# Kernel optimization log

Hardware: AMD Instinct MI355X
Metric: run time of the kernel (lower is better)

The kernel has to match this reference:

```python
import jax, jax.numpy as jnp
import numpy as np

DIM = 1024
HEADS = 16
HEAD_DIM = DIM // HEADS
FFN = 4 * DIM
EPS = 1e-5


def layer_norm(x, g, b):
    mu = jnp.mean(x, axis=-1, keepdims=True)
    var = jnp.mean(jnp.square(x - mu), axis=-1, keepdims=True)
    return (x - mu) * jax.lax.rsqrt(var + EPS) * g + b


def setup_inputs() -> dict:
    key = jax.random.key(0)
    ks = jax.random.split(key, 12)
    s_d = 1.0 / np.sqrt(DIM)
    s_f = 1.0 / np.sqrt(FFN)
    return {
        "x": jax.random.normal(ks[0], (2, 2048, DIM), dtype=jnp.float32),
        "ln1_g": jnp.ones((DIM,), jnp.float32),
        "ln1_b": jnp.zeros((DIM,), jnp.float32),
        "q_w": jax.random.normal(ks[1], (DIM, DIM), jnp.float32) * s_d,
        "k_w": jax.random.normal(ks[2], (DIM, DIM), jnp.float32) * s_d,
        "v_w": jax.random.normal(ks[3], (DIM, DIM), jnp.float32) * s_d,
        "o_w": jax.random.normal(ks[4], (DIM, DIM), jnp.float32) * s_d,
        "ln2_g": jnp.ones((DIM,), jnp.float32),
        "ln2_b": jnp.zeros((DIM,), jnp.float32),
        "ffn_in_w": jax.random.normal(ks[5], (FFN, DIM), jnp.float32) * s_d,
        "ffn_in_b": jnp.zeros((FFN,), jnp.float32),
        "sw_w": jax.random.normal(ks[6], (FFN, FFN), jnp.float32) * s_f,
        "sw_v": jax.random.normal(ks[7], (FFN, FFN), jnp.float32) * s_f,
        "ffn_out_w": jax.random.normal(ks[8], (DIM, FFN), jnp.float32) * s_f,
        "ffn_out_b": jnp.zeros((DIM,), jnp.float32),
    }


def reference(x, ln1_g, ln1_b, q_w, k_w, v_w, o_w, ln2_g, ln2_b,
              ffn_in_w, ffn_in_b, sw_w, sw_v, ffn_out_w, ffn_out_b):
    B, L, D = x.shape
    scale = HEAD_DIM ** -0.5

    # --- attention block ---
    h = layer_norm(x, ln1_g, ln1_b)
    q = (h @ q_w.T).reshape(B, L, HEADS, HEAD_DIM).transpose(0, 2, 1, 3)
    k = (h @ k_w.T).reshape(B, L, HEADS, HEAD_DIM).transpose(0, 2, 1, 3)
    v = (h @ v_w.T).reshape(B, L, HEADS, HEAD_DIM).transpose(0, 2, 1, 3)
    attn = jnp.einsum("bhqd,bhkd->bhqk", q, k) * scale
    attn = jax.nn.softmax(attn, axis=-1)
    out = jnp.einsum("bhqk,bhkd->bhqd", attn, v)
    out = out.transpose(0, 2, 1, 3).reshape(B, L, D)
    x = x + out @ o_w.T

    # --- FFN block: Linear -> SwiGLU -> Linear ---
    h = layer_norm(x, ln2_g, ln2_b)
    u = h @ ffn_in_w.T + ffn_in_b                 # [B,L,FFN]
    g = jax.nn.silu(u @ sw_w.T) * (u @ sw_v.T)    # SwiGLU
    x = x + g @ ffn_out_w.T + ffn_out_b
    return x
```

## Files before the change

### kernel.cpp

```cpp
#include <hip/hip_runtime.h>
#include <hip/hip_bf16.h>

#define TOK 4096
#define DIM 1024
#define FFN_N 4096
#define SEQ 2048
#define HD 64

using short8 = __attribute__((ext_vector_type(8))) short;
using short4v = __attribute__((ext_vector_type(4))) short;
using f32x4 = __attribute__((ext_vector_type(4))) float;

__device__ __forceinline__ short f2b(float f){
  return __builtin_bit_cast(short, __float2bfloat16(f));
}
__device__ __forceinline__ float b2f(short s){
  return __bfloat162float(__builtin_bit_cast(__hip_bfloat16, s));
}
__device__ __forceinline__ unsigned cvtpk(float lo, float hi){
  unsigned r;
  asm("v_cvt_pk_bf16_f32 %0, %1, %2" : "=v"(r) : "v"(lo), "v"(hi));
  return r;
}

__device__ __forceinline__ void gl_lds16(const short* g, short* l){
  __builtin_amdgcn_global_load_lds(
      (const __attribute__((address_space(1))) unsigned int*)g,
      (__attribute__((address_space(3))) unsigned int*)l, 16, 0, 0);
}

#define BARRAW() asm volatile("s_barrier" ::: "memory")
#define VMCNT(n) asm volatile("s_waitcnt vmcnt(" #n ")" ::: "memory")

__global__ __launch_bounds__(256) void castk(const float* __restrict__ src,
                                             short* __restrict__ dst, int n){
  int stride = gridDim.x*256*4;
  for (int i = (blockIdx.x*256 + threadIdx.x)*4; i < n; i += stride){
    float4 v = *reinterpret_cast<const float4*>(src + i);
    short4v o; o[0]=f2b(v.x); o[1]=f2b(v.y); o[2]=f2b(v.z); o[3]=f2b(v.w);
    *reinterpret_cast<short4v*>(dst + i) = o;
  }
}

__global__ __launch_bounds__(256) void lnk(const float* __restrict__ x,
                                           const float* __restrict__ g,
                                           const float* __restrict__ b,
                                           short* __restrict__ out){
  int row = blockIdx.x;
  int t = threadIdx.x;
  const float* xr = x + (size_t)row*DIM;
  float4 v = *reinterpret_cast<const float4*>(xr + t*4);
  float s = v.x+v.y+v.z+v.w;
  float s2 = v.x*v.x+v.y*v.y+v.z*v.z+v.w*v.w;
  #pragma unroll
  for (int off=1; off<64; off<<=1){ s += __shfl_xor(s,off); s2 += __shfl_xor(s2,off); }
  __shared__ float as_[4], as2_[4];
  if ((t&63)==0){ as_[t>>6]=s; as2_[t>>6]=s2; }
  __syncthreads();
  s = as_[0]+as_[1]+as_[2]+as_[3];
  s2 = as2_[0]+as2_[1]+as2_[2]+as2_[3];
  float mu = s * (1.0f/DIM);
  float var = s2 * (1.0f/DIM) - mu*mu;
  float r = rsqrtf(var + 1e-5f);
  float4 gv = *reinterpret_cast<const float4*>(g + t*4);
  float4 bv = *reinterpret_cast<const float4*>(b + t*4);
  short4v o;
  o[0]=f2b((v.x-mu)*r*gv.x + bv.x);
  o[1]=f2b((v.y-mu)*r*gv.y + bv.y);
  o[2]=f2b((v.z-mu)*r*gv.z + bv.z);
  o[3]=f2b((v.w-mu)*r*gv.w + bv.w);
  *reinterpret_cast<short4v*>(out + (size_t)row*DIM + t*4) = o;
}

template<int MODE>
__global__ __launch_bounds__(256,2) void gemm_bt(
    const short* __restrict__ A, const short* __restrict__ Bt,
    short* __restrict__ Cb, float* __restrict__ Cf,
    const float* __restrict__ bias, const float* __restrict__ resid,
    const short* __restrict__ aux,
    int M, int N, int K)
{
  __shared__ __align__(16) short Al[128*32];
  __shared__ __align__(16) short Bl[128*32];
  const int tid = threadIdx.x, lane = tid & 63, w = tid >> 6;
  const int wr = w >> 1, wc = w & 1;
  const int bx = blockIdx.x, by = blockIdx.y;

  const short* ga0 = A  + (size_t)(by*128 + w*32 + (lane>>2))*K + (lane&3)*8;
  const short* gb0 = Bt + (size_t)(bx*128 + w*32 + (lane>>2))*K + (lane&3)*8;
  short* la0 = &Al[w*32*32];
  short* lb0 = &Bl[w*32*32];

  f32x4 acc[4][4] = {};

  for (int k0 = 0; k0 < K; k0 += 32){
    __syncthreads();
    gl_lds16(ga0 + k0,                 la0);
    gl_lds16(ga0 + k0 + (size_t)16*K,  la0 + 16*32);
    gl_lds16(gb0 + k0,                 lb0);
    gl_lds16(gb0 + k0 + (size_t)16*K,  lb0 + 16*32);
    __syncthreads();
    short8 af[4], bf[4];
    #pragma unroll
    for (int m=0;m<4;m++)
      af[m] = *reinterpret_cast<const short8*>(&Al[(wr*64 + m*16 + (lane&15))*32 + (lane>>4)*8]);
    #pragma unroll
    for (int n=0;n<4;n++)
      bf[n] = *reinterpret_cast<const short8*>(&Bl[(wc*64 + n*16 + (lane&15))*32 + (lane>>4)*8]);
    #pragma unroll
    for (int m=0;m<4;m++)
      #pragma unroll
      for (int n=0;n<4;n++)
        acc[m][n] = __builtin_amdgcn_mfma_f32_16x16x32_bf16(af[m], bf[n], acc[m][n], 0,0,0);
  }

  #pragma unroll
  for (int m=0;m<4;m++){
    #pragma unroll
    for (int n=0;n<4;n++){
      #pragma unroll
      for (int j=0;j<4;j++){
        int r = by*128 + wr*64 + m*16 + ((lane>>4)<<2) + j;
        int c = bx*128 + wc*64 + n*16 + (lane&15);
        float v = acc[m][n][j];
        if (MODE==1 || MODE==3) v += bias[c];
        size_t idx = (size_t)r*N + c;
        if (MODE==4){
          float a = b2f(aux[idx]);
          float sg = a / (1.0f + __expf(-a));
          Cb[idx] = f2b(sg * v);
        } else if (MODE<=1) {
          Cb[idx] = f2b(v);
        } else {
          Cf[idx] = resid[idx] + v;
        }
      }
    }
  }
}

template<int MODE>
__global__ __launch_bounds__(512,2) void gemm256(
    const short* __restrict__ A, const short* __restrict__ Bt,
    short* __restrict__ Cb,
    const float* __restrict__ bias, const short* __restrict__ aux,
    int M, int N, int K)
{
  __shared__ __align__(16) short L[65536];
  const int tid = threadIdx.x, lane = tid&63, w = tid>>6;
  const int q15 = lane&15, h8 = lane>>4;
  const int wm = w>>2, wn = w&3;
  const int NT = K>>6;

  int bid = blockIdx.x;
  int wg = (bid&7)*(gridDim.x>>3) + (bid>>3);
  const int by = wg >> 4, bx = wg & 15;

  const int isub = w*8 + (lane>>3);
  const int koff = ((lane&7) ^ ((lane>>3)&7))*8;

  const short* gA[2][2]; const short* gB[2][2];
  #pragma unroll
  for (int hh=0; hh<2; hh++){
    #pragma unroll
    for (int j=0; j<2; j++){
      int i = j*64 + isub;
      int Ra = by*256 + (i>>6)*128 + hh*64 + (i&63);
      gA[hh][j] = A + (size_t)Ra*K + koff;
      int Rb = bx*256 + (i>>5)*64 + hh*32 + (i&31);
      gB[hh][j] = Bt + (size_t)Rb*K + koff;
    }
  }

  auto stA = [&](int db, int hh, int j, int kt){
    gl_lds16(gA[hh][j] + (size_t)kt*64, &L[db*32768 + hh*8192 + j*4096 + w*512]);
  };
  auto stB = [&](int db, int hh, int j, int kt){
    gl_lds16(gB[hh][j] + (size_t)kt*64, &L[db*32768 + (2+hh)*8192 + j*4096 + w*512]);
  };
  auto rdA = [&](int db, int mh, int m, int ks)->short8{
    int i = wm*64 + m*16 + q15;
    int ch = (ks*4 + h8) ^ (i&7);
    return *reinterpret_cast<const short8*>(&L[db*32768 + mh*8192 + i*64 + ch*8]);
  };
  auto rdB = [&](int db, int nh, int n, int ks)->short8{
    int i = wn*32 + n*16 + q15;
    int ch = (ks*4 + h8) ^ (i&7);
    return *reinterpret_cast<const short8*>(&L[db*32768 + (2+nh)*8192 + i*64 + ch*8]);
  };

  f32x4 acc[8][4] = {};
  short8 af[4][2], bf[2][2];

#define MFMA_QUAD(MH, NH)                                                      \
  __builtin_amdgcn_s_setprio(1);                                               \
  _Pragma("unroll")                                                            \
  for (int m=0;m<4;m++){                                                       \
    _Pragma("unroll")                                                          \
    for (int n=0;n<2;n++){                                                     \
      acc[(MH)*4+m][(NH)*2+n] = __builtin_amdgcn_mfma_f32_16x16x32_bf16(       \
          af[m][0], bf[n][0], acc[(MH)*4+m][(NH)*2+n], 0,0,0);                 \
      acc[(MH)*4+m][(NH)*2+n] = __builtin_amdgcn_mfma_f32_16x16x32_bf16(       \
          af[m][1], bf[n][1], acc[(MH)*4+m][(NH)*2+n], 0,0,0);                 \
    }                                                                          \
  }                                                                            \
  __builtin_amdgcn_s_setprio(0);

  stA(0,0,0,0); stA(0,0,1,0);
  stB(0,0,0,0); stB(0,0,1,0);
  stA(0,1,0,0); stA(0,1,1,0);
  stB(0,1,0,0); stB(0,1,1,0);
  VMCNT(4);
  BARRAW();

  for (int t = 0; t < NT; ++t){
    const int db = t&1;
    const bool pf = (t+1 < NT);

    #pragma unroll
    for (int m=0;m<4;m++){ af[m][0]=rdA(db,0,m,0); af[m][1]=rdA(db,0,m,1); }
    #pragma unroll
    for (int n=0;n<2;n++){ bf[n][0]=rdB(db,0,n,0); bf[n][1]=rdB(db,0,n,1); }
    if (pf){ stA(db^1,0,0,t+1); stA(db^1,0,1,t+1); }
    BARRAW();
    MFMA_QUAD(0,0);
    if (pf){ VMCNT(2); } else { VMCNT(0); }
    BARRAW();

    #pragma unroll
    for (int n=0;n<2;n++){ bf[n][0]=rdB(db,1,n,0); bf[n][1]=rdB(db,1,n,1); }
    if (pf){ stB(db^1,0,0,t+1); stB(db^1,0,1,t+1); }
    BARRAW();
    MFMA_QUAD(0,1);
    BARRAW();

    #pragma unroll
    for (int m=0;m<4;m++){ af[m][0]=rdA(db,1,m,0); af[m][1]=rdA(db,1,m,1); }
    if (pf){ stA(db^1,1,0,t+1); stA(db^1,1,1,t+1); }
    BARRAW();
    MFMA_QUAD(1,1);
    BARRAW();

    #pragma unroll
    for (int n=0;n<2;n++){ bf[n][0]=rdB(db,0,n,0); bf[n][1]=rdB(db,0,n,1); }
    if (pf){ stB(db^1,1,0,t+1); stB(db^1,1,1,t+1); }
    BARRAW();
    MFMA_QUAD(1,0);
    if (pf){ VMCNT(4); }
    BARRAW();
  }

  #pragma unroll
  for (int mq=0;mq<8;mq++){
    #pragma unroll
    for (int nq=0;nq<4;nq++){
      #pragma unroll
      for (int jj=0;jj<4;jj++){
        int r = by*256 + wm*128 + mq*16 + h8*4 + jj;
        int c = bx*256 + wn*64  + nq*16 + q15;
        float v = acc[mq][nq][jj];
        if (MODE==1) v += bias[c];
        size_t idx = (size_t)r*N + c;
        if (MODE==4){
          float a = b2f(aux[idx]);
          float sg = a / (1.0f + __expf(-a));
          Cb[idx] = f2b(sg * v);
        } else {
          Cb[idx] = f2b(v);
        }
      }
    }
  }
#undef MFMA_QUAD
}

__global__ __launch_bounds__(256) void vtrk(const short* __restrict__ V,
                                            short* __restrict__ Vt){
  __shared__ __align__(16) short T[64*72];
  const int tid = threadIdx.x;
  const int bh = blockIdx.y;
  const int b = bh >> 4, hd = bh & 15;
  const int t0 = blockIdx.x * 64;
  const short* src = V + (size_t)b*SEQ*DIM + (size_t)hd*HD;

  const int r = tid>>2, c = tid&3;
  short8 a0 = *reinterpret_cast<const short8*>(src + (size_t)(t0+r)*DIM + c*8);
  short8 a1 = *reinterpret_cast<const short8*>(src + (size_t)(t0+r)*DIM + (c+4)*8);
  *reinterpret_cast<short8*>(&T[r*72 + c*8]) = a0;
  *reinterpret_cast<short8*>(&T[r*72 + (c+4)*8]) = a1;
  __syncthreads();

  short* dst = Vt + (size_t)bh*HD*SEQ;
  #pragma unroll
  for (int dd=0; dd<2; dd++){
    int d = (tid>>3) + dd*32;
    int tc = tid&7;
    short8 o;
    #pragma unroll
    for (int j=0;j<8;j++) o[j] = T[(tc*8+j)*72 + d];
    *reinterpret_cast<short8*>(dst + (size_t)d*SEQ + t0 + tc*8) = o;
  }
}

__global__ __launch_bounds__(256) void attnk(
    const short* __restrict__ Q, const short* __restrict__ K,
    const short* __restrict__ Vt, short* __restrict__ O)
{
  __shared__ __align__(16) short Kl[64*64];
  __shared__ __align__(16) short Vl[64*64];
  __shared__ __align__(16) short Pl[4*16*72];

  const int tid = threadIdx.x, lane = tid&63, w = tid>>6;
  const int h = lane>>4, q15 = lane&15;
  const int bh = blockIdx.y;
  const int b = bh >> 4, hd = bh & 15;
  const int q0 = blockIdx.x * 64;
  const size_t base = (size_t)b*SEQ*DIM + (size_t)hd*HD;
  const size_t vbase = (size_t)bh*HD*SEQ;

  short8 aq[2];
  {
    int qrow = q0 + w*16 + q15;
    const short* qp = Q + base + (size_t)qrow*DIM + h*8;
    aq[0] = *reinterpret_cast<const short8*>(qp);
    aq[1] = *reinterpret_cast<const short8*>(qp + 32);
  }

  float mrun = -1e30f, lrun = 0.f;
  f32x4 o[4] = {};

  const int ksub = lane>>3;
  const int kchunk = (lane&7) ^ ksub;
  const short* kg0 = K + base + (size_t)(w*16 + ksub)*DIM + kchunk*8;
  const short* kg1 = kg0 + (size_t)8*DIM;
  const short* vg0 = Vt + vbase + (size_t)(w*16 + ksub)*SEQ + kchunk*8;
  const short* vg1 = vg0 + (size_t)8*SEQ;
  short* kl0 = &Kl[(w*16)*64];
  short* kl1 = &Kl[(w*16 + 8)*64];
  short* vl0 = &Vl[(w*16)*64];
  short* vl1 = &Vl[(w*16 + 8)*64];

  short* plw = &Pl[w*16*72];
  const int xk = (q15&7);

  for (int kv0 = 0; kv0 < SEQ; kv0 += 64){
    __syncthreads();
    gl_lds16(kg0 + (size_t)kv0*DIM, kl0);
    gl_lds16(kg1 + (size_t)kv0*DIM, kl1);
    gl_lds16(vg0 + kv0, vl0);
    gl_lds16(vg1 + kv0, vl1);
    __syncthreads();

    f32x4 s[4];
    #pragma unroll
    for (int nt=0; nt<4; nt++){
      const short8 kf0 = *reinterpret_cast<const short8*>(
          &Kl[(nt*16+q15)*64 + ((h    ^ xk)*8)]);
      const short8 kf1 = *reinterpret_cast<const short8*>(
          &Kl[(nt*16+q15)*64 + (((4+h)^ xk)*8)]);
      f32x4 t = {};
      t = __builtin_amdgcn_mfma_f32_16x16x32_bf16(kf0, aq[0], t, 0,0,0);
      t = __builtin_amdgcn_mfma_f32_16x16x32_bf16(kf1, aq[1], t, 0,0,0);
      s[nt] = t * 0.125f;
    }

    float pm = s[0][0];
    #pragma unroll
    for (int nt=0; nt<4; nt++)
      #pragma unroll
      for (int j=0; j<4; j++) pm = fmaxf(pm, s[nt][j]);
    pm = fmaxf(pm, __shfl_xor(pm, 16));
    pm = fmaxf(pm, __shfl_xor(pm, 32));

    float mn = fmaxf(mrun, pm);
    float al = __expf(mrun - mn);
    mrun = mn;
    float rs = 0.f;
    #pragma unroll
    for (int nt=0; nt<4; nt++)
      #pragma unroll
      for (int j=0; j<4; j++){
        s[nt][j] = __expf(s[nt][j] - mn);
        rs += s[nt][j];
      }
    rs += __shfl_xor(rs, 16);
    rs += __shfl_xor(rs, 32);
    lrun = lrun*al + rs;

    float alj[4];
    #pragma unroll
    for (int j=0;j<4;j++) alj[j] = __shfl(al, 4*h + j);
    #pragma unroll
    for (int dt=0;dt<4;dt++)
      #pragma unroll
      for (int j=0;j<4;j++) o[dt][j] *= alj[j];

    #pragma unroll
    for (int nt=0;nt<4;nt++){
      uint2 u;
      u.x = cvtpk(s[nt][0], s[nt][1]);
      u.y = cvtpk(s[nt][2], s[nt][3]);
      *reinterpret_cast<uint2*>(&plw[q15*72 + nt*16 + 4*h]) = u;
    }
    asm volatile("s_waitcnt lgkmcnt(0)" ::: "memory");
    const short8 ap0 = *reinterpret_cast<const short8*>(&plw[q15*72 +      h*8]);
    const short8 ap1 = *reinterpret_cast<const short8*>(&plw[q15*72 + 32 + h*8]);

    #pragma unroll
    for (int dt=0;dt<4;dt++){
      const short8 vf0 = *reinterpret_cast<const short8*>(
          &Vl[(dt*16+q15)*64 + ((h    ^ xk)*8)]);
      const short8 vf1 = *reinterpret_cast<const short8*>(
          &Vl[(dt*16+q15)*64 + (((4+h)^ xk)*8)]);
      o[dt] = __builtin_amdgcn_mfma_f32_16x16x32_bf16(ap0, vf0, o[dt], 0,0,0);
      o[dt] = __builtin_amdgcn_mfma_f32_16x16x32_bf16(ap1, vf1, o[dt], 0,0,0);
    }
  }

  float rl[4];
  #pragma unroll
  for (int j=0;j<4;j++) rl[j] = 1.0f / __shfl(lrun, 4*h + j);
  #pragma unroll
  for (int dt=0;dt<4;dt++)
    #pragma unroll
    for (int j=0;j<4;j++){
      int qrow = q0 + w*16 + 4*h + j;
      O[base + (size_t)qrow*DIM + dt*16 + q15] = f2b(o[dt][j]*rl[j]);
    }
}

extern "C" void kernel_launch(void* const* d_in, const int* in_sizes, int n_in,
                              void* d_out, int out_size, void* d_ws, size_t ws_size,
                              hipStream_t stream) {
  const float* x     = (const float*)d_in[0];
  const float* ln1_g = (const float*)d_in[1];
  const float* ln1_b = (const float*)d_in[2];
  const float* q_w   = (const float*)d_in[3];
  const float* k_w   = (const float*)d_in[4];
  const float* v_w   = (const float*)d_in[5];
  const float* o_w   = (const float*)d_in[6];
  const float* ln2_g = (const float*)d_in[7];
  const float* ln2_b = (const float*)d_in[8];
  const float* fi_w  = (const float*)d_in[9];
  const float* fi_b  = (const float*)d_in[10];
  const float* sw_w  = (const float*)d_in[11];
  const float* sw_v  = (const float*)d_in[12];
  const float* fo_w  = (const float*)d_in[13];
  const float* fo_b  = (const float*)d_in[14];
  float* out = (float*)d_out;

  char* W = (char*)d_ws;
  const size_t MB = 1024*1024;
  short* qw  = (short*)(W +   0*MB);
  short* kw  = (short*)(W +   2*MB);
  short* vw  = (short*)(W +   4*MB);
  short* ow  = (short*)(W +   6*MB);
  short* fiw = (short*)(W +   8*MB);
  short* sww = (short*)(W +  16*MB);
  short* swv = (short*)(W +  48*MB);
  short* fow = (short*)(W +  80*MB);
  short* hb  = (short*)(W +  88*MB);
  short* qb  = (short*)(W +  96*MB);
  short* kb  = (short*)(W + 104*MB);
  short* vb  = (short*)(W + 112*MB);
  short* ab  = (short*)(W + 120*MB);
  float* x2  = (float*)(W + 128*MB);
  short* ub  = (short*)(W + 144*MB);
  short* gb  = (short*)(W + 176*MB);
  short* a1  = (short*)(W +  96*MB);
  short* vt  = (short*)(W + 144*MB);

  dim3 blk(256);
  castk<<<1024,blk,0,stream>>>(q_w, qw, 1024*1024);
  castk<<<1024,blk,0,stream>>>(k_w, kw, 1024*1024);
  castk<<<1024,blk,0,stream>>>(v_w, vw, 1024*1024);
  castk<<<1024,blk,0,stream>>>(o_w, ow, 1024*1024);
  castk<<<2048,blk,0,stream>>>(fi_w, fiw, 4096*1024);
  castk<<<2048,blk,0,stream>>>(sw_w, sww, 4096*4096);
  castk<<<2048,blk,0,stream>>>(sw_v, swv, 4096*4096);
  castk<<<2048,blk,0,stream>>>(fo_w, fow, 1024*4096);

  lnk<<<TOK,blk,0,stream>>>(x, ln1_g, ln1_b, hb);
  gemm_bt<0><<<dim3(8,32),blk,0,stream>>>(hb, qw, qb, nullptr, nullptr, nullptr, nullptr, TOK, DIM, DIM);
  gemm_bt<0><<<dim3(8,32),blk,0,stream>>>(hb, kw, kb, nullptr, nullptr, nullptr, nullptr, TOK, DIM, DIM);
  gemm_bt<0><<<dim3(8,32),blk,0,stream>>>(hb, vw, vb, nullptr, nullptr, nullptr, nullptr, TOK, DIM, DIM);
  vtrk<<<dim3(SEQ/64,32),blk,0,stream>>>(vb, vt);
  attnk<<<dim3(32,32),blk,0,stream>>>(qb, kb, vt, ab);
  gemm_bt<2><<<dim3(8,32),blk,0,stream>>>(ab, ow, nullptr, x2, nullptr, x, nullptr, TOK, DIM, DIM);
  lnk<<<TOK,blk,0,stream>>>(x2, ln2_g, ln2_b, hb);
  gemm256<1><<<256, 512, 0, stream>>>(hb, fiw, ub, fi_b, nullptr, TOK, FFN_N, DIM);
  gemm256<0><<<256, 512, 0, stream>>>(ub, sww, a1, nullptr, nullptr, TOK, FFN_N, FFN_N);
  gemm256<4><<<256, 512, 0, stream>>>(ub, swv, gb, nullptr, a1, TOK, FFN_N, FFN_N);
  gemm_bt<3><<<dim3(8,32),blk,0,stream>>>(gb, fow, nullptr, out, fo_b, x2, nullptr, TOK, DIM, FFN_N);
}
```

Before: 627.3 us.

## Keep both B fragment halves in registers and front-load next-tile global prefetches

Each B half's fragments now stay in separate register sets (bf0/bf1), so the fourth MFMA quadrant reuses bf0 instead of re-reading it from LDS. The global-to-LDS prefetches for the next k-tile are issued in two groups in the first two phases rather than spread over four. This cuts LDS reads per iteration and issues global loads earlier to hide more latency. In exchange it uses more VGPRs for fragments, which may lower occupancy, and the vmcnt waits are changed, so the ordering between loads and barriers has to stay correct.

```diff
diff --git a/kernel.cpp b/kernel.cpp
--- a/kernel.cpp
+++ b/kernel.cpp
@@ -190,18 +190,18 @@
   };
 
   f32x4 acc[8][4] = {};
-  short8 af[4][2], bf[2][2];
-
-#define MFMA_QUAD(MH, NH)                                                      \
+  short8 af[4][2], bf0[2][2], bf1[2][2];
+
+#define MFMA_QUAD(MH, NH, BF)                                                  \
   __builtin_amdgcn_s_setprio(1);                                               \
   _Pragma("unroll")                                                            \
   for (int m=0;m<4;m++){                                                       \
     _Pragma("unroll")                                                          \
     for (int n=0;n<2;n++){                                                     \
       acc[(MH)*4+m][(NH)*2+n] = __builtin_amdgcn_mfma_f32_16x16x32_bf16(       \
-          af[m][0], bf[n][0], acc[(MH)*4+m][(NH)*2+n], 0,0,0);                 \
+          af[m][0], BF[n][0], acc[(MH)*4+m][(NH)*2+n], 0,0,0);                 \
       acc[(MH)*4+m][(NH)*2+n] = __builtin_amdgcn_mfma_f32_16x16x32_bf16(       \
-          af[m][1], bf[n][1], acc[(MH)*4+m][(NH)*2+n], 0,0,0);                 \
+          af[m][1], BF[n][1], acc[(MH)*4+m][(NH)*2+n], 0,0,0);                 \
     }                                                                          \
   }                                                                            \
   __builtin_amdgcn_s_setprio(0);
@@ -220,33 +220,31 @@
     #pragma unroll
     for (int m=0;m<4;m++){ af[m][0]=rdA(db,0,m,0); af[m][1]=rdA(db,0,m,1); }
     #pragma unroll
-    for (int n=0;n<2;n++){ bf[n][0]=rdB(db,0,n,0); bf[n][1]=rdB(db,0,n,1); }
-    if (pf){ stA(db^1,0,0,t+1); stA(db^1,0,1,t+1); }
-    BARRAW();
-    MFMA_QUAD(0,0);
-    if (pf){ VMCNT(2); } else { VMCNT(0); }
-    BARRAW();
-
-    #pragma unroll
-    for (int n=0;n<2;n++){ bf[n][0]=rdB(db,1,n,0); bf[n][1]=rdB(db,1,n,1); }
-    if (pf){ stB(db^1,0,0,t+1); stB(db^1,0,1,t+1); }
-    BARRAW();
-    MFMA_QUAD(0,1);
+    for (int n=0;n<2;n++){ bf0[n][0]=rdB(db,0,n,0); bf0[n][1]=rdB(db,0,n,1); }
+    if (pf){ stA(db^1,0,0,t+1); stA(db^1,0,1,t+1);
+             stB(db^1,0,0,t+1); stB(db^1,0,1,t+1); }
+    BARRAW();
+    MFMA_QUAD(0,0,bf0);
+    if (pf){ VMCNT(4); } else { VMCNT(0); }
+    BARRAW();
+
+    #pragma unroll
+    for (int n=0;n<2;n++){ bf1[n][0]=rdB(db,1,n,0); bf1[n][1]=rdB(db,1,n,1); }
+    if (pf){ stA(db^1,1,0,t+1); stA(db^1,1,1,t+1);
+             stB(db^1,1,0,t+1); stB(db^1,1,1,t+1); }
+    BARRAW();
+    MFMA_QUAD(0,1,bf1);
     BARRAW();
 
     #pragma unroll
     for (int m=0;m<4;m++){ af[m][0]=rdA(db,1,m,0); af[m][1]=rdA(db,1,m,1); }
-    if (pf){ stA(db^1,1,0,t+1); stA(db^1,1,1,t+1); }
-    BARRAW();
-    MFMA_QUAD(1,1);
-    BARRAW();
-
-    #pragma unroll
-    for (int n=0;n<2;n++){ bf[n][0]=rdB(db,0,n,0); bf[n][1]=rdB(db,0,n,1); }
-    if (pf){ stB(db^1,1,0,t+1); stB(db^1,1,1,t+1); }
-    BARRAW();
-    MFMA_QUAD(1,0);
-    if (pf){ VMCNT(4); }
+    BARRAW();
+    MFMA_QUAD(1,1,bf1);
+    BARRAW();
+
+    BARRAW();
+    MFMA_QUAD(1,0,bf0);
+    if (pf){ VMCNT(4); } else { VMCNT(0); }
     BARRAW();
   }
 
```

Result: slower. 647.4 us (+3.2%).
